# Kernel optimization log

Hardware: AMD Instinct MI355X
Metric: run time of the kernel (lower is better)

The kernel has to match this reference:

```python
import jax, jax.numpy as jnp
import numpy as np

B, D_IN, HID, LAT, K = 8192, 1024, 2048, 256, 4096

def setup_inputs() -> dict:
    key = jax.random.key(0)
    ks = jax.random.split(key, 16)
    s = lambda fan_in: 1.0 / np.sqrt(fan_in)
    inp = {
        'x':  jax.random.normal(ks[0], (B, D_IN), jnp.float32),
        # encoder MLP
        'W1': jax.random.normal(ks[1], (D_IN, HID), jnp.float32) * s(D_IN),
        'b1': jnp.zeros((HID,), jnp.float32),
        'W2': jax.random.normal(ks[2], (HID, HID), jnp.float32) * s(HID),
        'b2': jnp.zeros((HID,), jnp.float32),
        'W3': jax.random.normal(ks[3], (HID, LAT), jnp.float32) * s(HID),
        'b3': jnp.zeros((LAT,), jnp.float32),
        # codebook, uniform(-1/K, 1/K) per nn.init.uniform_
        'embed': jax.random.uniform(ks[4], (K, LAT), jnp.float32, -1.0 / K, 1.0 / K),
        # decoder MLP
        'D1': jax.random.normal(ks[5], (LAT, HID), jnp.float32) * s(LAT),
        'd1': jnp.zeros((HID,), jnp.float32),
        'D2': jax.random.normal(ks[6], (HID, HID), jnp.float32) * s(HID),
        'd2': jnp.zeros((HID,), jnp.float32),
        'D3': jax.random.normal(ks[7], (HID, D_IN), jnp.float32) * s(HID),
        'd3': jnp.zeros((D_IN,), jnp.float32),
    }
    return inp

def gelu(x):
    return jax.nn.gelu(x, approximate=False)  # torch nn.GELU default is exact erf

def reference(x, W1, b1, W2, b2, W3, b3, embed, D1, d1, D2, d2, D3, d3):
    sg = jax.lax.stop_gradient
    # encoder: [B, D_in] -> [B, latent]
    h = gelu(x @ W1 + b1)
    h = gelu(h @ W2 + b2)
    z_e = h @ W3 + b3
    # squared distances to codebook: ||z||^2 + ||e||^2 - 2 z.e -> [B, K]
    z_sq = jnp.sum(z_e * z_e, axis=1, keepdims=True)
    e_sq = jnp.sum(embed * embed, axis=1)[None, :]
    dist = z_sq + e_sq - 2.0 * (z_e @ embed.T)
    indices = jnp.argmin(dist, axis=1)            # [B]
    z_q = embed[indices]                          # [B, latent]
    commitment = jnp.mean((z_e - sg(z_q)) ** 2)
    codebook = jnp.mean((z_q - sg(z_e)) ** 2)
    vq_loss = codebook + 0.25 * commitment
    # straight-through estimator
    z_st = z_e + sg(z_q - z_e)
    # decoder: [B, latent] -> [B, D_in]
    g = gelu(z_st @ D1 + d1)
    g = gelu(g @ D2 + d2)
    x_recon = g @ D3 + d3
    return x_recon, vq_loss, indices
```

## Files before the change

### kernel.cpp

```cpp
#include <hip/hip_runtime.h>
#include <math.h>

#define B_    8192
#define DIN_  1024
#define HID_  2048
#define LAT_  256
#define KC_   4096

using bfrag8 = __attribute__((ext_vector_type(8))) short;
using short8 = __attribute__((ext_vector_type(8))) short;
using half8  = __attribute__((ext_vector_type(8))) _Float16;
using facc4  = __attribute__((ext_vector_type(4))) float;

__device__ __forceinline__ unsigned short f2bf(float f) {
    union { float f; unsigned int u; } c; c.f = f;
    unsigned int u = c.u;
    return (unsigned short)((u + 0x7FFFu + ((u >> 16) & 1u)) >> 16);
}

__device__ __forceinline__ unsigned short f2h_bits(float f) {
    union { _Float16 h; unsigned short u; } c; c.h = (_Float16)f;
    return c.u;
}

template <int GELU, int OUT_SPLIT>
__global__ __launch_bounds__(256, 2) void gemm_split_f16(
    const unsigned short* __restrict__ Ahi, const unsigned short* __restrict__ Alo,
    const unsigned short* __restrict__ WThi, const unsigned short* __restrict__ WTlo,
    const float* __restrict__ bias,
    unsigned short* __restrict__ Chi, unsigned short* __restrict__ Clo,
    float* __restrict__ Cf32,
    int M, int N, int K)
{
    __shared__ __align__(16) unsigned short AsH[128 * 64];
    __shared__ __align__(16) unsigned short AsL[128 * 64];
    __shared__ __align__(16) unsigned short WsH[64 * 64];
    __shared__ __align__(16) unsigned short WsL[64 * 64];

    const int tid  = threadIdx.x;
    const int wave = tid >> 6;
    const int lane = tid & 63;
    const int wm   = wave & 1;
    const int wn   = wave >> 1;
    const int quad = lane >> 4;
    const int ln   = lane & 15;
    const int n0 = blockIdx.x * 64;
    const int m0 = blockIdx.y * 128;

    const facc4 fz4 = {0.0f, 0.0f, 0.0f, 0.0f};
    facc4 accA[4][2] = {};
    facc4 accB[4][2] = {};
    facc4 master[4][2] = {};

    for (int k0 = 0; k0 < K; k0 += 64) {
#pragma unroll
        for (int i = 0; i < 4; ++i) {
            const int idx = i * 256 + tid;
            const int row = idx >> 3;
            const int g   = idx & 7;
            const int dst = row * 64 + ((g ^ (row & 7)) << 3);
            const size_t src = (size_t)(m0 + row) * K + k0 + g * 8;
            *reinterpret_cast<short8*>(&AsH[dst]) =
                *reinterpret_cast<const short8*>(&Ahi[src]);
            *reinterpret_cast<short8*>(&AsL[dst]) =
                *reinterpret_cast<const short8*>(&Alo[src]);
        }
#pragma unroll
        for (int i = 0; i < 2; ++i) {
            const int idx = i * 256 + tid;
            const int row = idx >> 3;
            const int g   = idx & 7;
            const int dst = row * 64 + ((g ^ (row & 7)) << 3);
            const size_t src = (size_t)(n0 + row) * K + k0 + g * 8;
            *reinterpret_cast<short8*>(&WsH[dst]) =
                *reinterpret_cast<const short8*>(&WThi[src]);
            *reinterpret_cast<short8*>(&WsL[dst]) =
                *reinterpret_cast<const short8*>(&WTlo[src]);
        }
        __syncthreads();
#pragma unroll
        for (int ks = 0; ks < 64; ks += 32) {
            const int gq = (ks >> 3) + quad;
            half8 aH[4], aL[4], bH[2], bL[2];
#pragma unroll
            for (int f = 0; f < 4; ++f) {
                const int row = wm * 64 + f * 16 + ln;
                const int off = row * 64 + ((gq ^ (ln & 7)) << 3);
                aH[f] = *reinterpret_cast<const half8*>(&AsH[off]);
                aL[f] = *reinterpret_cast<const half8*>(&AsL[off]);
            }
#pragma unroll
            for (int f = 0; f < 2; ++f) {
                const int row = wn * 32 + f * 16 + ln;
                const int off = row * 64 + ((gq ^ (ln & 7)) << 3);
                bH[f] = *reinterpret_cast<const half8*>(&WsH[off]);
                bL[f] = *reinterpret_cast<const half8*>(&WsL[off]);
            }
#pragma unroll
            for (int fm = 0; fm < 4; ++fm)
#pragma unroll
                for (int fn = 0; fn < 2; ++fn)
                    accA[fm][fn] = __builtin_amdgcn_mfma_f32_16x16x32_f16(
                        aH[fm], bH[fn], accA[fm][fn], 0, 0, 0);
#pragma unroll
            for (int fm = 0; fm < 4; ++fm)
#pragma unroll
                for (int fn = 0; fn < 2; ++fn)
                    accB[fm][fn] = __builtin_amdgcn_mfma_f32_16x16x32_f16(
                        aH[fm], bL[fn], accB[fm][fn], 0, 0, 0);
#pragma unroll
            for (int fm = 0; fm < 4; ++fm)
#pragma unroll
                for (int fn = 0; fn < 2; ++fn)
                    accB[fm][fn] = __builtin_amdgcn_mfma_f32_16x16x32_f16(
                        aL[fm], bH[fn], accB[fm][fn], 0, 0, 0);
        }
        __syncthreads();
        if ((k0 & 192) == 192) {
#pragma unroll
            for (int fm = 0; fm < 4; ++fm)
#pragma unroll
                for (int fn = 0; fn < 2; ++fn) {
                    master[fm][fn] += accA[fm][fn];
                    accA[fm][fn] = fz4;
                }
        }
    }

    const double SC_HI = 0.015625;
    const double SC_LO = 3.814697265625e-06;
#pragma unroll
    for (int fn = 0; fn < 2; ++fn) {
        const int col = n0 + wn * 32 + fn * 16 + ln;
        const double bb = (double)bias[col];
#pragma unroll
        for (int fm = 0; fm < 4; ++fm) {
            const int rbase = m0 + wm * 64 + fm * 16 + quad * 4;
#pragma unroll
            for (int r = 0; r < 4; ++r) {
                double v = (double)master[fm][fn][r] * SC_HI
                         + (double)accB[fm][fn][r] * SC_LO + bb;
                if (GELU) v = 0.5 * v * (1.0 + erf(v * 0.70710678118654752440));
                if (OUT_SPLIT) {
                    const float hf = (float)v;
                    const _Float16 hi = (_Float16)hf;
                    const float lo = ((float)hf - (float)hi) * 4096.0f;
                    union { _Float16 h; unsigned short u; } c1, c2;
                    c1.h = hi; c2.h = (_Float16)lo;
                    Chi[(size_t)(rbase + r) * N + col] = c1.u;
                    Clo[(size_t)(rbase + r) * N + col] = c2.u;
                } else {
                    Cf32[(size_t)(rbase + r) * N + col] = (float)v;
                }
            }
        }
    }
}

__global__ __launch_bounds__(256) void split_scaled_f16x2(
    const float* __restrict__ X, unsigned short* __restrict__ Xhi,
    unsigned short* __restrict__ Xlo, int n4, float scale)
{
    const int i = blockIdx.x * 256 + threadIdx.x;
    if (i >= n4) return;
    const float4 v = reinterpret_cast<const float4*>(X)[i];
    ushort4 h, l;
    {
        const float s = v.x * scale;
        _Float16 a = (_Float16)s; h.x = f2h_bits((float)a); l.x = f2h_bits((s - (float)a) * 4096.0f);
    }
    {
        const float s = v.y * scale;
        _Float16 a = (_Float16)s; h.y = f2h_bits((float)a); l.y = f2h_bits((s - (float)a) * 4096.0f);
    }
    {
        const float s = v.z * scale;
        _Float16 a = (_Float16)s; h.z = f2h_bits((float)a); l.z = f2h_bits((s - (float)a) * 4096.0f);
    }
    {
        const float s = v.w * scale;
        _Float16 a = (_Float16)s; h.w = f2h_bits((float)a); l.w = f2h_bits((s - (float)a) * 4096.0f);
    }
    reinterpret_cast<ushort4*>(Xhi)[i] = h;
    reinterpret_cast<ushort4*>(Xlo)[i] = l;
}

__global__ __launch_bounds__(256) void wsplit_transpose(
    const float* __restrict__ W, unsigned short* __restrict__ WThi,
    unsigned short* __restrict__ WTlo, int K, int N)
{
    __shared__ float t[32][33];
    const int k0 = blockIdx.x * 32;
    const int n0 = blockIdx.y * 32;
    const int x = threadIdx.x;
    const int y = threadIdx.y;
#pragma unroll
    for (int i = 0; i < 4; ++i)
        t[y + i * 8][x] = W[(size_t)(k0 + y + i * 8) * N + n0 + x];
    __syncthreads();
#pragma unroll
    for (int i = 0; i < 4; ++i) {
        const float w = t[x][y + i * 8] * 64.0f;
        const _Float16 hi = (_Float16)w;
        const float lo = (w - (float)hi) * 4096.0f;
        WThi[(size_t)(n0 + y + i * 8) * K + k0 + x] = f2h_bits((float)hi);
        WTlo[(size_t)(n0 + y + i * 8) * K + k0 + x] = f2h_bits(lo);
    }
}

__global__ __launch_bounds__(256, 2) void vq_argmin_mfma(
    const unsigned short* __restrict__ Zhi, const unsigned short* __restrict__ Zlo,
    const unsigned short* __restrict__ Ehi, const unsigned short* __restrict__ Elo,
    const float* __restrict__ esq, const float* __restrict__ zsq,
    float* __restrict__ pval, int* __restrict__ pidx)
{
    __shared__ __align__(16) unsigned short ZsH[128 * 64];
    __shared__ __align__(16) unsigned short ZsL[128 * 64];
    __shared__ __align__(16) unsigned short EsH[64 * 64];
    __shared__ __align__(16) unsigned short EsL[64 * 64];
    __shared__ float rbv[128][2];
    __shared__ int   rbi[128][2];

    const int tid  = threadIdx.x;
    const int wave = tid >> 6;
    const int lane = tid & 63;
    const int wm   = wave & 1;
    const int wn   = wave >> 1;
    const int quad = lane >> 4;
    const int ln   = lane & 15;
    const int m0    = blockIdx.x * 128;
    const int split = blockIdx.y;

    const double SC_A = 1.52587890625e-05;
    const double SC_B = 3.725290298461914e-09;

    float bestv[4][4];
    int   besti[4][4];
#pragma unroll
    for (int a = 0; a < 4; ++a)
#pragma unroll
        for (int b = 0; b < 4; ++b) { bestv[a][b] = 3.4e38f; besti[a][b] = 0; }

    for (int nt = 0; nt < 8; ++nt) {
        const int n0 = split * 512 + nt * 64;
        facc4 accA[4][2] = {};
        facc4 accB[4][2] = {};
        for (int k0 = 0; k0 < 256; k0 += 64) {
            __syncthreads();
#pragma unroll
            for (int i = 0; i < 4; ++i) {
                const int idx = i * 256 + tid;
                const int row = idx >> 3;
                const int g   = idx & 7;
                const int dst = row * 64 + ((g ^ (row & 7)) << 3);
                const size_t src = (size_t)(m0 + row) * LAT_ + k0 + g * 8;
                *reinterpret_cast<short8*>(&ZsH[dst]) =
                    *reinterpret_cast<const short8*>(&Zhi[src]);
                *reinterpret_cast<short8*>(&ZsL[dst]) =
                    *reinterpret_cast<const short8*>(&Zlo[src]);
            }
#pragma unroll
            for (int i = 0; i < 2; ++i) {
                const int idx = i * 256 + tid;
                const int row = idx >> 3;
                const int g   = idx & 7;
                const int dst = row * 64 + ((g ^ (row & 7)) << 3);
                const size_t src = (size_t)(n0 + row) * LAT_ + k0 + g * 8;
                *reinterpret_cast<short8*>(&EsH[dst]) =
                    *reinterpret_cast<const short8*>(&Ehi[src]);
                *reinterpret_cast<short8*>(&EsL[dst]) =
                    *reinterpret_cast<const short8*>(&Elo[src]);
            }
            __syncthreads();
#pragma unroll
            for (int ks = 0; ks < 64; ks += 32) {
                const int gq = (ks >> 3) + quad;
                half8 aH[4], aL[4], bH[2], bL[2];
#pragma unroll
                for (int f = 0; f < 4; ++f) {
                    const int row = wm * 64 + f * 16 + ln;
                    const int off = row * 64 + ((gq ^ (ln & 7)) << 3);
                    aH[f] = *reinterpret_cast<const half8*>(&ZsH[off]);
                    aL[f] = *reinterpret_cast<const half8*>(&ZsL[off]);
                }
#pragma unroll
                for (int f = 0; f < 2; ++f) {
                    const int row = wn * 32 + f * 16 + ln;
                    const int off = row * 64 + ((gq ^ (ln & 7)) << 3);
                    bH[f] = *reinterpret_cast<const half8*>(&EsH[off]);
                    bL[f] = *reinterpret_cast<const half8*>(&EsL[off]);
                }
#pragma unroll
                for (int fm = 0; fm < 4; ++fm)
#pragma unroll
                    for (int fn = 0; fn < 2; ++fn)
                        accA[fm][fn] = __builtin_amdgcn_mfma_f32_16x16x32_f16(
                            aH[fm], bH[fn], accA[fm][fn], 0, 0, 0);
#pragma unroll
                for (int fm = 0; fm < 4; ++fm)
#pragma unroll
                    for (int fn = 0; fn < 2; ++fn)
                        accB[fm][fn] = __builtin_amdgcn_mfma_f32_16x16x32_f16(
                            aH[fm], bL[fn], accB[fm][fn], 0, 0, 0);
#pragma unroll
                for (int fm = 0; fm < 4; ++fm)
#pragma unroll
                    for (int fn = 0; fn < 2; ++fn)
                        accB[fm][fn] = __builtin_amdgcn_mfma_f32_16x16x32_f16(
                            aL[fm], bH[fn], accB[fm][fn], 0, 0, 0);
            }
        }
#pragma unroll
        for (int fm = 0; fm < 4; ++fm) {
            const float4 zq4 = *reinterpret_cast<const float4*>(
                &zsq[m0 + wm * 64 + fm * 16 + quad * 4]);
#pragma unroll
            for (int r = 0; r < 4; ++r) {
                float v0 = 3.4e38f; int i0 = 0;
#pragma unroll
                for (int fn = 0; fn < 2; ++fn) {
                    const int n = n0 + wn * 32 + fn * 16 + ln;
                    const float es = esq[n];
                    const float S = ((const float*)&zq4)[r] + es;
                    const double d = (double)accA[fm][fn][r] * SC_A
                                   + (double)accB[fm][fn][r] * SC_B;
                    const float t2m = (float)(2.0 * d);
                    const float sc = S - t2m;
                    if (sc < v0 || (sc == v0 && n < i0)) { v0 = sc; i0 = n; }
                }
#pragma unroll
                for (int mask = 1; mask < 16; mask <<= 1) {
                    const float v2 = __shfl_xor(v0, mask, 64);
                    const int   i2 = __shfl_xor(i0, mask, 64);
                    if (v2 < v0 || (v2 == v0 && i2 < i0)) { v0 = v2; i0 = i2; }
                }
                if (v0 < bestv[fm][r] || (v0 == bestv[fm][r] && i0 < besti[fm][r])) {
                    bestv[fm][r] = v0; besti[fm][r] = i0;
                }
            }
        }
    }

    if (ln == 0) {
#pragma unroll
        for (int fm = 0; fm < 4; ++fm)
#pragma unroll
            for (int r = 0; r < 4; ++r) {
                const int rl = wm * 64 + fm * 16 + quad * 4 + r;
                rbv[rl][wn] = bestv[fm][r];
                rbi[rl][wn] = besti[fm][r];
            }
    }
    __syncthreads();
    if (tid < 128) {
        float bv = rbv[tid][0]; int bi = rbi[tid][0];
        const float v = rbv[tid][1]; const int ix = rbi[tid][1];
        if (v < bv || (v == bv && ix < bi)) { bv = v; bi = ix; }
        pval[(size_t)(m0 + tid) * 8 + split] = bv;
        pidx[(m0 + tid) * 8 + split] = bi;
    }
}

template <int OUT_BF16>
__global__ __launch_bounds__(256) void gemm_mfma_bf16(
    const unsigned short* __restrict__ A,
    const unsigned short* __restrict__ WT,
    const float* __restrict__ bias,
    void* __restrict__ Cout,
    int M, int N, int K)
{
    __shared__ unsigned short As[128 * 64];
    __shared__ unsigned short Bs[128 * 64];

    const int tid  = threadIdx.x;
    const int wave = tid >> 6;
    const int lane = tid & 63;
    const int wm   = wave & 1;
    const int wn   = wave >> 1;
    const int quad = lane >> 4;
    const int ln   = lane & 15;
    const int m0 = blockIdx.x * 128;
    const int n0 = blockIdx.y * 128;

    facc4 acc[4][4] = {};

    for (int k0 = 0; k0 < K; k0 += 64) {
#pragma unroll
        for (int i = 0; i < 4; ++i) {
            const int idx = i * 256 + tid;
            const int row = idx >> 3;
            const int c8  = (idx & 7) * 8;
            *reinterpret_cast<bfrag8*>(&As[row * 64 + c8]) =
                *reinterpret_cast<const bfrag8*>(&A[(size_t)(m0 + row) * K + k0 + c8]);
            *reinterpret_cast<bfrag8*>(&Bs[row * 64 + c8]) =
                *reinterpret_cast<const bfrag8*>(&WT[(size_t)(n0 + row) * K + k0 + c8]);
        }
        __syncthreads();
#pragma unroll
        for (int ks = 0; ks < 64; ks += 32) {
            bfrag8 am[4], bn[4];
#pragma unroll
            for (int f = 0; f < 4; ++f) {
                am[f] = *reinterpret_cast<const bfrag8*>(
                    &As[(wm * 64 + f * 16 + ln) * 64 + ks + quad * 8]);
                bn[f] = *reinterpret_cast<const bfrag8*>(
                    &Bs[(wn * 64 + f * 16 + ln) * 64 + ks + quad * 8]);
            }
#pragma unroll
            for (int fm = 0; fm < 4; ++fm)
#pragma unroll
                for (int fn = 0; fn < 4; ++fn)
                    acc[fm][fn] = __builtin_amdgcn_mfma_f32_16x16x32_bf16(
                        am[fm], bn[fn], acc[fm][fn], 0, 0, 0);
        }
        __syncthreads();
    }

#pragma unroll
    for (int fn = 0; fn < 4; ++fn) {
        const int col = n0 + wn * 64 + fn * 16 + ln;
        const float bf = bias[col];
#pragma unroll
        for (int fm = 0; fm < 4; ++fm) {
            const int rbase = m0 + wm * 64 + fm * 16 + quad * 4;
#pragma unroll
            for (int r = 0; r < 4; ++r) {
                float v = acc[fm][fn][r] + bf;
                if (OUT_BF16) {
                    v = 0.5f * v * (1.0f + erff(v * 0.70710678118654752440f));
                    ((unsigned short*)Cout)[(size_t)(rbase + r) * N + col] = f2bf(v);
                } else {
                    ((float*)Cout)[(size_t)(rbase + r) * N + col] = v;
                }
            }
        }
    }
}

__global__ __launch_bounds__(256) void cast_transpose_w(
    const float* __restrict__ W, unsigned short* __restrict__ WT, int K, int N)
{
    __shared__ float t[32][33];
    const int k0 = blockIdx.x * 32;
    const int n0 = blockIdx.y * 32;
    const int x = threadIdx.x;
    const int y = threadIdx.y;
#pragma unroll
    for (int i = 0; i < 4; ++i)
        t[y + i * 8][x] = W[(size_t)(k0 + y + i * 8) * N + n0 + x];
    __syncthreads();
#pragma unroll
    for (int i = 0; i < 4; ++i)
        WT[(size_t)(n0 + y + i * 8) * K + k0 + x] = f2bf(t[x][y + i * 8]);
}

__global__ __launch_bounds__(64) void rowsq_kernel(
    const float* __restrict__ X, float* __restrict__ out,
    float* __restrict__ loss_slot)
{
    const int r = blockIdx.x;
    const float4 v = reinterpret_cast<const float4*>(X + (size_t)r * LAT_)[threadIdx.x];
    double s = (double)v.x * v.x + (double)v.y * v.y + (double)v.z * v.z + (double)v.w * v.w;
#pragma unroll
    for (int off = 32; off; off >>= 1) s += __shfl_down(s, off, 64);
    if (threadIdx.x == 0) {
        out[r] = (float)s;
        if (loss_slot != nullptr && r == 0) *loss_slot = 0.0f;
    }
}

__global__ __launch_bounds__(64) void vq_finalize(
    const float* __restrict__ pval, const int* __restrict__ pidx,
    const float* __restrict__ Z, const float* __restrict__ E,
    unsigned short* __restrict__ zqb, float* __restrict__ out_idx,
    float* __restrict__ loss_slot)
{
    const int row = blockIdx.x;
    __shared__ int sidx;
    if (threadIdx.x == 0) {
        float bv = pval[row * 8]; int bi = pidx[row * 8];
#pragma unroll
        for (int s = 1; s < 8; ++s) {
            const float v = pval[row * 8 + s]; const int ix = pidx[row * 8 + s];
            if (v < bv || (v == bv && ix < bi)) { bv = v; bi = ix; }
        }
        sidx = bi;
        out_idx[row] = (float)bi;
    }
    __syncthreads();
    const int idx = sidx;
    const float4 e = reinterpret_cast<const float4*>(E + (size_t)idx * LAT_)[threadIdx.x];
    const float4 z = reinterpret_cast<const float4*>(Z + (size_t)row * LAT_)[threadIdx.x];
    ushort4 q; q.x = f2bf(e.x); q.y = f2bf(e.y); q.z = f2bf(e.z); q.w = f2bf(e.w);
    reinterpret_cast<ushort4*>(zqb + (size_t)row * LAT_)[threadIdx.x] = q;
    const float dx = z.x - e.x, dy = z.y - e.y, dz = z.z - e.z, dw = z.w - e.w;
    float s = dx * dx + dy * dy + dz * dz + dw * dw;
#pragma unroll
    for (int off = 32; off; off >>= 1) s += __shfl_down(s, off, 64);
    if (threadIdx.x == 0)
        atomicAdd(loss_slot, s * (1.25f / ((float)B_ * (float)LAT_)));
}

extern "C" void kernel_launch(void* const* d_in, const int* in_sizes, int n_in,
                              void* d_out, int out_size, void* d_ws, size_t ws_size,
                              hipStream_t stream)
{
    const float* x   = (const float*)d_in[0];
    const float* W1  = (const float*)d_in[1];
    const float* b1  = (const float*)d_in[2];
    const float* W2  = (const float*)d_in[3];
    const float* b2  = (const float*)d_in[4];
    const float* W3  = (const float*)d_in[5];
    const float* b3  = (const float*)d_in[6];
    const float* emb = (const float*)d_in[7];
    const float* D1  = (const float*)d_in[8];
    const float* d1  = (const float*)d_in[9];
    const float* D2  = (const float*)d_in[10];
    const float* d2  = (const float*)d_in[11];
    const float* D3  = (const float*)d_in[12];
    const float* d3  = (const float*)d_in[13];
    float* out = (float*)d_out;

    char* ws = (char*)d_ws;
    const size_t MB = 1u << 20;
    unsigned short* h1hi = (unsigned short*)(ws);
    unsigned short* h1lo = (unsigned short*)(ws + 32 * MB);
    unsigned short* zehi = (unsigned short*)(ws);
    unsigned short* zelo = (unsigned short*)(ws + 4 * MB);
    unsigned short* g1b  = (unsigned short*)(ws);
    unsigned short* zqb  = (unsigned short*)(ws + 32 * MB);
    unsigned short* g2b  = (unsigned short*)(ws + 32 * MB);
    unsigned short* xhi  = (unsigned short*)(ws + 64 * MB);
    unsigned short* xlo  = (unsigned short*)(ws + 80 * MB);
    unsigned short* h2hi = (unsigned short*)(ws + 64 * MB);
    unsigned short* h2lo = (unsigned short*)(ws + 96 * MB);
    unsigned short* wt1  = (unsigned short*)(ws + 64 * MB);
    unsigned short* wt2  = (unsigned short*)(ws + 65 * MB);
    unsigned short* wt3  = (unsigned short*)(ws + 73 * MB);
    float* ze = (float*)(ws + 128 * MB);
    unsigned short* w1thi = (unsigned short*)(ws + 136 * MB);
    unsigned short* w1tlo = (unsigned short*)(ws + 140 * MB);
    unsigned short* w2thi = (unsigned short*)(ws + 136 * MB);
    unsigned short* w2tlo = (unsigned short*)(ws + 144 * MB);
    unsigned short* w3thi = (unsigned short*)(ws + 136 * MB);
    unsigned short* w3tlo = (unsigned short*)(ws + 137 * MB);
    unsigned short* ehi   = (unsigned short*)(ws + 144 * MB);
    unsigned short* elo   = (unsigned short*)(ws + 146 * MB);
    float* esq  = (float*)(ws + 152 * MB);
    float* zsq  = (float*)(ws + 152 * MB + 64 * 1024);
    float* pval = (float*)(ws + 152 * MB + 128 * 1024);
    int*   pidx = (int*)  (ws + 152 * MB + 384 * 1024);

    float* loss_slot = out + (size_t)B_ * DIN_;
    float* out_idx   = loss_slot + 1;

    rowsq_kernel<<<KC_, 64, 0, stream>>>(emb, esq, loss_slot);

    split_scaled_f16x2<<<(B_ * DIN_ / 4 + 255) / 256, 256, 0, stream>>>(
        x, xhi, xlo, B_ * DIN_ / 4, 1.0f);
    wsplit_transpose<<<dim3(DIN_ / 32, HID_ / 32), dim3(32, 8), 0, stream>>>(W1, w1thi, w1tlo, DIN_, HID_);

    gemm_split_f16<1, 1><<<dim3(HID_ / 64, B_ / 128), 256, 0, stream>>>(
        xhi, xlo, w1thi, w1tlo, b1, h1hi, h1lo, nullptr, B_, HID_, DIN_);

    wsplit_transpose<<<dim3(HID_ / 32, HID_ / 32), dim3(32, 8), 0, stream>>>(W2, w2thi, w2tlo, HID_, HID_);

    gemm_split_f16<1, 1><<<dim3(HID_ / 64, B_ / 128), 256, 0, stream>>>(
        h1hi, h1lo, w2thi, w2tlo, b2, h2hi, h2lo, nullptr, B_, HID_, HID_);

    split_scaled_f16x2<<<(KC_ * LAT_ / 4 + 255) / 256, 256, 0, stream>>>(
        emb, ehi, elo, KC_ * LAT_ / 4, 65536.0f);
    wsplit_transpose<<<dim3(HID_ / 32, LAT_ / 32), dim3(32, 8), 0, stream>>>(W3, w3thi, w3tlo, HID_, LAT_);

    gemm_split_f16<0, 0><<<dim3(LAT_ / 64, B_ / 128), 256, 0, stream>>>(
        h2hi, h2lo, w3thi, w3tlo, b3, nullptr, nullptr, ze, B_, LAT_, HID_);

    split_scaled_f16x2<<<(B_ * LAT_ / 4 + 255) / 256, 256, 0, stream>>>(
        ze, zehi, zelo, B_ * LAT_ / 4, 1.0f);
    rowsq_kernel<<<B_, 64, 0, stream>>>(ze, zsq, nullptr);

    cast_transpose_w<<<dim3(LAT_ / 32, HID_ / 32), dim3(32, 8), 0, stream>>>(D1, wt1, LAT_, HID_);
    cast_transpose_w<<<dim3(HID_ / 32, HID_ / 32), dim3(32, 8), 0, stream>>>(D2, wt2, HID_, HID_);
    cast_transpose_w<<<dim3(HID_ / 32, DIN_ / 32), dim3(32, 8), 0, stream>>>(D3, wt3, HID_, DIN_);

    vq_argmin_mfma<<<dim3(B_ / 128, 8), 256, 0, stream>>>(
        zehi, zelo, ehi, elo, esq, zsq, pval, pidx);
    vq_finalize<<<B_, 64, 0, stream>>>(pval, pidx, ze, emb, zqb, out_idx, loss_slot);

    gemm_mfma_bf16<1><<<dim3(B_ / 128, HID_ / 128), 256, 0, stream>>>(zqb, wt1, d1, (void*)g1b, B_, HID_, LAT_);
    gemm_mfma_bf16<1><<<dim3(B_ / 128, HID_ / 128), 256, 0, stream>>>(g1b, wt2, d2, (void*)g2b, B_, HID_, HID_);
    gemm_mfma_bf16<0><<<dim3(B_ / 128, DIN_ / 128), 256, 0, stream>>>(g2b, wt3, d3, (void*)out, B_, DIN_, HID_);
}
```

Before: 1.146 ms.

## Load GEMM tiles directly into LDS and fuse z_e split into GEMM epilogue

Replaces the register-staged global-to-shared tile copies in the split-f16 GEMM, the VQ argmin kernel and the bf16 GEMM with global_load_lds direct-to-LDS loads. The XOR swizzle moves from the destination address to the source address. The third encoder GEMM now writes both the fp32 z_e and its hi/lo f16 split, so the separate split kernel is dropped. Launch bounds on the split GEMM are raised to 3 blocks per SIMD, which may cause register spills in exchange for higher occupancy.

```diff
diff --git a/kernel.cpp b/kernel.cpp
--- a/kernel.cpp
+++ b/kernel.cpp
@@ -23,8 +23,14 @@
     return c.u;
 }
 
+__device__ __forceinline__ void gload16(const unsigned short* g, unsigned short* l) {
+    __builtin_amdgcn_global_load_lds(
+        (const __attribute__((address_space(1))) void*)(g),
+        (__attribute__((address_space(3))) void*)(l), 16, 0, 0);
+}
+
 template <int GELU, int OUT_SPLIT>
-__global__ __launch_bounds__(256, 2) void gemm_split_f16(
+__global__ __launch_bounds__(256, 3) void gemm_split_f16(
     const unsigned short* __restrict__ Ahi, const unsigned short* __restrict__ Alo,
     const unsigned short* __restrict__ WThi, const unsigned short* __restrict__ WTlo,
     const float* __restrict__ bias,
@@ -57,25 +63,21 @@
         for (int i = 0; i < 4; ++i) {
             const int idx = i * 256 + tid;
             const int row = idx >> 3;
-            const int g   = idx & 7;
-            const int dst = row * 64 + ((g ^ (row & 7)) << 3);
-            const size_t src = (size_t)(m0 + row) * K + k0 + g * 8;
-            *reinterpret_cast<short8*>(&AsH[dst]) =
-                *reinterpret_cast<const short8*>(&Ahi[src]);
-            *reinterpret_cast<short8*>(&AsL[dst]) =
-                *reinterpret_cast<const short8*>(&Alo[src]);
+            const int gs  = (idx & 7) ^ (row & 7);
+            const int wb  = i * 256 + (tid & 192);
+            const size_t src = (size_t)(m0 + row) * K + k0 + gs * 8;
+            gload16(&Ahi[src], &AsH[wb * 8]);
+            gload16(&Alo[src], &AsL[wb * 8]);
         }
 #pragma unroll
         for (int i = 0; i < 2; ++i) {
             const int idx = i * 256 + tid;
             const int row = idx >> 3;
-            const int g   = idx & 7;
-            const int dst = row * 64 + ((g ^ (row & 7)) << 3);
-            const size_t src = (size_t)(n0 + row) * K + k0 + g * 8;
-            *reinterpret_cast<short8*>(&WsH[dst]) =
-                *reinterpret_cast<const short8*>(&WThi[src]);
-            *reinterpret_cast<short8*>(&WsL[dst]) =
-                *reinterpret_cast<const short8*>(&WTlo[src]);
+            const int gs  = (idx & 7) ^ (row & 7);
+            const int wb  = i * 256 + (tid & 192);
+            const size_t src = (size_t)(n0 + row) * K + k0 + gs * 8;
+            gload16(&WThi[src], &WsH[wb * 8]);
+            gload16(&WTlo[src], &WsL[wb * 8]);
         }
         __syncthreads();
 #pragma unroll
@@ -141,16 +143,17 @@
                 double v = (double)master[fm][fn][r] * SC_HI
                          + (double)accB[fm][fn][r] * SC_LO + bb;
                 if (GELU) v = 0.5 * v * (1.0 + erf(v * 0.70710678118654752440));
-                if (OUT_SPLIT) {
-                    const float hf = (float)v;
+                const float hf = (float)v;
+                if (OUT_SPLIT == 1 || OUT_SPLIT == 2) {
                     const _Float16 hi = (_Float16)hf;
-                    const float lo = ((float)hf - (float)hi) * 4096.0f;
+                    const float lo = (hf - (float)hi) * 4096.0f;
                     union { _Float16 h; unsigned short u; } c1, c2;
                     c1.h = hi; c2.h = (_Float16)lo;
                     Chi[(size_t)(rbase + r) * N + col] = c1.u;
                     Clo[(size_t)(rbase + r) * N + col] = c2.u;
-                } else {
-                    Cf32[(size_t)(rbase + r) * N + col] = (float)v;
+                }
+                if (OUT_SPLIT == 0 || OUT_SPLIT == 2) {
+                    Cf32[(size_t)(rbase + r) * N + col] = hf;
                 }
             }
         }
@@ -251,25 +254,21 @@
             for (int i = 0; i < 4; ++i) {
                 const int idx = i * 256 + tid;
                 const int row = idx >> 3;
-                const int g   = idx & 7;
-                const int dst = row * 64 + ((g ^ (row & 7)) << 3);
-                const size_t src = (size_t)(m0 + row) * LAT_ + k0 + g * 8;
-                *reinterpret_cast<short8*>(&ZsH[dst]) =
-                    *reinterpret_cast<const short8*>(&Zhi[src]);
-                *reinterpret_cast<short8*>(&ZsL[dst]) =
-                    *reinterpret_cast<const short8*>(&Zlo[src]);
+                const int gs  = (idx & 7) ^ (row & 7);
+                const int wb  = i * 256 + (tid & 192);
+                const size_t src = (size_t)(m0 + row) * LAT_ + k0 + gs * 8;
+                gload16(&Zhi[src], &ZsH[wb * 8]);
+                gload16(&Zlo[src], &ZsL[wb * 8]);
             }
 #pragma unroll
             for (int i = 0; i < 2; ++i) {
                 const int idx = i * 256 + tid;
                 const int row = idx >> 3;
-                const int g   = idx & 7;
-                const int dst = row * 64 + ((g ^ (row & 7)) << 3);
-                const size_t src = (size_t)(n0 + row) * LAT_ + k0 + g * 8;
-                *reinterpret_cast<short8*>(&EsH[dst]) =
-                    *reinterpret_cast<const short8*>(&Ehi[src]);
-                *reinterpret_cast<short8*>(&EsL[dst]) =
-                    *reinterpret_cast<const short8*>(&Elo[src]);
+                const int gs  = (idx & 7) ^ (row & 7);
+                const int wb  = i * 256 + (tid & 192);
+                const size_t src = (size_t)(n0 + row) * LAT_ + k0 + gs * 8;
+                gload16(&Ehi[src], &EsH[wb * 8]);
+                gload16(&Elo[src], &EsL[wb * 8]);
             }
             __syncthreads();
 #pragma unroll
@@ -369,8 +368,8 @@
     void* __restrict__ Cout,
     int M, int N, int K)
 {
-    __shared__ unsigned short As[128 * 64];
-    __shared__ unsigned short Bs[128 * 64];
+    __shared__ __align__(16) unsigned short As[128 * 64];
+    __shared__ __align__(16) unsigned short Bs[128 * 64];
 
     const int tid  = threadIdx.x;
     const int wave = tid >> 6;
@@ -390,10 +389,9 @@
             const int idx = i * 256 + tid;
             const int row = idx >> 3;
             const int c8  = (idx & 7) * 8;
-            *reinterpret_cast<bfrag8*>(&As[row * 64 + c8]) =
-                *reinterpret_cast<const bfrag8*>(&A[(size_t)(m0 + row) * K + k0 + c8]);
-            *reinterpret_cast<bfrag8*>(&Bs[row * 64 + c8]) =
-                *reinterpret_cast<const bfrag8*>(&WT[(size_t)(n0 + row) * K + k0 + c8]);
+            const int wb  = i * 256 + (tid & 192);
+            gload16(&A[(size_t)(m0 + row) * K + k0 + c8], &As[wb * 8]);
+            gload16(&WT[(size_t)(n0 + row) * K + k0 + c8], &Bs[wb * 8]);
         }
         __syncthreads();
 #pragma unroll
@@ -572,11 +570,9 @@
         emb, ehi, elo, KC_ * LAT_ / 4, 65536.0f);
     wsplit_transpose<<<dim3(HID_ / 32, LAT_ / 32), dim3(32, 8), 0, stream>>>(W3, w3thi, w3tlo, HID_, LAT_);
 
-    gemm_split_f16<0, 0><<<dim3(LAT_ / 64, B_ / 128), 256, 0, stream>>>(
-        h2hi, h2lo, w3thi, w3tlo, b3, nullptr, nullptr, ze, B_, LAT_, HID_);
-
-    split_scaled_f16x2<<<(B_ * LAT_ / 4 + 255) / 256, 256, 0, stream>>>(
-        ze, zehi, zelo, B_ * LAT_ / 4, 1.0f);
+    gemm_split_f16<0, 2><<<dim3(LAT_ / 64, B_ / 128), 256, 0, stream>>>(
+        h2hi, h2lo, w3thi, w3tlo, b3, zehi, zelo, ze, B_, LAT_, HID_);
+
     rowsq_kernel<<<B_, 64, 0, stream>>>(ze, zsq, nullptr);
 
     cast_transpose_w<<<dim3(LAT_ / 32, HID_ / 32), dim3(32, 8), 0, stream>>>(D1, wt1, LAT_, HID_);
```

Measured after the change: 1.097 ms. 1.04x faster.
